# Kernel optimization log

Hardware: AMD Instinct MI355X
Metric: run time of the kernel (lower is better)

Reference implementation:

```python
import jax, jax.numpy as jnp
import numpy as np

EMB_DIM = 512
CATE1_CNT = 10
VOCAB = 100000
H_D = 1024
BN_EPS = 1e-5
NEG = -1e30  # masked value for max-pool


def setup_inputs() -> dict:
    key = jax.random.key(0)
    ks = jax.random.split(key, 12)
    B, LT, LD = 1024, 50, 200
    title = jax.random.randint(ks[0], (B, LT), 0, VOCAB, dtype=jnp.int64)
    desc = jax.random.randint(ks[1], (B, LD), 0, VOCAB, dtype=jnp.int64)
    t_len = jax.random.randint(ks[2], (B,), 1, LT + 1, dtype=jnp.int64)
    d_len = jax.random.randint(ks[3], (B,), 1, LD + 1, dtype=jnp.int64)
    emb = jax.random.normal(ks[4], (VOCAB, EMB_DIM), dtype=jnp.float32) * 0.02
    W_fc = jax.random.normal(ks[5], (4 * EMB_DIM, H_D), dtype=jnp.float32) * (1.0 / np.sqrt(4 * EMB_DIM))
    b_fc = jnp.zeros((H_D,), dtype=jnp.float32)
    gamma = jnp.ones((H_D,), dtype=jnp.float32)
    beta = jnp.zeros((H_D,), dtype=jnp.float32)
    W_clf = jax.random.normal(ks[6], (H_D, CATE1_CNT), dtype=jnp.float32) * (1.0 / np.sqrt(H_D))
    b_clf = jnp.zeros((CATE1_CNT,), dtype=jnp.float32)
    return {"title": title, "desc": desc, "t_len": t_len, "d_len": d_len,
            "emb": emb, "W_fc": W_fc, "b_fc": b_fc, "gamma": gamma,
            "beta": beta, "W_clf": W_clf, "b_clf": b_clf}


def _swem_pool(tokens, lens, emb):
    # tokens: [B, L] int, lens: [B] int -> (avg, max) each [B, D]
    e = emb[tokens]                                   # [B, L, D] gather
    L = tokens.shape[1]
    mask = (jnp.arange(L)[None, :] < lens[:, None])[..., None]  # [B, L, 1]
    s = jnp.sum(jnp.where(mask, e, 0.0), axis=1)      # [B, D]
    avg = s / jnp.maximum(lens, 1).astype(e.dtype)[:, None]
    mx = jnp.max(jnp.where(mask, e, NEG), axis=1)     # [B, D]
    return avg, mx


def reference(title, desc, t_len, d_len, emb, W_fc, b_fc, gamma, beta, W_clf, b_clf):
    t_avg, t_max = _swem_pool(title, t_len, emb)
    d_avg, d_max = _swem_pool(desc, d_len, emb)
    swem = jnp.concatenate([t_avg, t_max, d_avg, d_max], axis=-1)  # [B, 2048]
    h = swem @ W_fc + b_fc                                         # [B, H_D]
    # BatchNorm1d in training mode: batch statistics
    mean = jnp.mean(h, axis=0)
    var = jnp.var(h, axis=0)
    h = (h - mean) * jax.lax.rsqrt(var + BN_EPS) * gamma + beta
    h = jax.nn.relu(h)
    return h @ W_clf + b_clf                                       # [B, 10]
```

## Files before the change

### kernel.cpp

```cpp
#include <hip/hip_runtime.h>
#include <hip/hip_bf16.h>

#define EMB_DIM 512
#define B_SZ 1024
#define LT 50
#define LD 200
#define H_D 1024
#define K_FC 2048
#define NCLS 10
#define BN_EPS 1e-5f
#define NEGV -1e30f

typedef short short8 __attribute__((ext_vector_type(8)));
typedef float f32x4 __attribute__((ext_vector_type(4)));

#define SWZ(r, b) ((b) ^ (((r) & 7) << 4))

#define ACC4(S, M, E) \
  S.x += E.x; S.y += E.y; S.z += E.z; S.w += E.w; \
  M.x = fmaxf(M.x, E.x); M.y = fmaxf(M.y, E.y); \
  M.z = fmaxf(M.z, E.z); M.w = fmaxf(M.w, E.w);

__global__ __launch_bounds__(512) void pool_tr_kernel(
    const int* __restrict__ title, const int* __restrict__ desc,
    const int* __restrict__ t_len, const int* __restrict__ d_len,
    const float* __restrict__ emb, __hip_bfloat16* __restrict__ swem,
    const float* __restrict__ W, __hip_bfloat16* __restrict__ Wt,
    const float* __restrict__ Wclf, float* __restrict__ WclfT) {
  __shared__ float sm[8192];
  __shared__ int idxs[264];

  const int bid = blockIdx.x;
  const int tid = threadIdx.x;

  if (bid >= 2 * B_SZ) {
    const int t = bid - 2 * B_SZ;
    if (t == 512) {
      for (int idx = tid; idx < NCLS * H_D; idx += 512) {
        int j = idx >> 10, k = idx & 1023;
        WclfT[j * H_D + k] = Wclf[(size_t)k * NCLS + j];
      }
      return;
    }
    const int n0 = (t & 15) * 64;
    const int k0 = (t >> 4) * 64;
#pragma unroll
    for (int i = 0; i < 8; ++i) {
      int idx = i * 512 + tid;
      int r = idx >> 6, c = idx & 63;
      sm[r * 65 + c] = W[(size_t)(k0 + r) * H_D + n0 + c];
    }
    __syncthreads();
#pragma unroll
    for (int i = 0; i < 8; ++i) {
      int idx = i * 512 + tid;
      int r = idx >> 6, c = idx & 63;
      Wt[(size_t)(n0 + r) * K_FC + k0 + c] = __float2bfloat16(sm[c * 65 + r]);
    }
    return;
  }

  const int b = bid >> 1;
  const int half = bid & 1;
  const int wave = tid >> 6;
  const int lane = tid & 63;
  const int dbase = half * 256 + lane * 4;

  if (tid < LT) idxs[tid] = title[b * LT + tid];
  else if (tid >= 64 && tid < 64 + LD) idxs[tid] = desc[b * LD + tid - 64];
  const int tl = t_len[b];
  const int dl = d_len[b];
  __syncthreads();

#define POOL_LIST(LEN, IDXOFF, SARR, MARR)                                         \
  {                                                                                \
    float4 s0 = make_float4(0.f, 0.f, 0.f, 0.f), s1 = s0;                          \
    float4 m0 = make_float4(NEGV, NEGV, NEGV, NEGV), m1 = m0;                      \
    const int cnt = (LEN > wave) ? ((LEN - wave + 7) >> 3) : 0;                    \
    if (cnt >= 2) {                                                                \
      float4 e0 = *reinterpret_cast<const float4*>(                                \
          emb + (size_t)idxs[IDXOFF + wave] * EMB_DIM + dbase);                    \
      float4 e1 = *reinterpret_cast<const float4*>(                                \
          emb + (size_t)idxs[IDXOFF + wave + 8] * EMB_DIM + dbase);                \
      int i = 2;                                                                   \
      for (; i + 1 < cnt; i += 2) {                                                \
        float4 n0 = *reinterpret_cast<const float4*>(                              \
            emb + (size_t)idxs[IDXOFF + wave + i * 8] * EMB_DIM + dbase);          \
        float4 n1 = *reinterpret_cast<const float4*>(                              \
            emb + (size_t)idxs[IDXOFF + wave + (i + 1) * 8] * EMB_DIM + dbase);    \
        ACC4(s0, m0, e0); ACC4(s1, m1, e1);                                        \
        e0 = n0; e1 = n1;                                                          \
      }                                                                            \
      ACC4(s0, m0, e0); ACC4(s1, m1, e1);                                          \
      if (i < cnt) {                                                               \
        float4 t2 = *reinterpret_cast<const float4*>(                              \
            emb + (size_t)idxs[IDXOFF + wave + i * 8] * EMB_DIM + dbase);          \
        ACC4(s0, m0, t2);                                                          \
      }                                                                            \
    } else if (cnt == 1) {                                                         \
      float4 e0 = *reinterpret_cast<const float4*>(                                \
          emb + (size_t)idxs[IDXOFF + wave] * EMB_DIM + dbase);                    \
      ACC4(s0, m0, e0);                                                            \
    }                                                                              \
    s0.x += s1.x; s0.y += s1.y; s0.z += s1.z; s0.w += s1.w;                        \
    m0.x = fmaxf(m0.x, m1.x); m0.y = fmaxf(m0.y, m1.y);                            \
    m0.z = fmaxf(m0.z, m1.z); m0.w = fmaxf(m0.w, m1.w);                            \
    *reinterpret_cast<float4*>(&sm[(SARR * 8 + wave) * 256 + lane * 4]) = s0;      \
    *reinterpret_cast<float4*>(&sm[(MARR * 8 + wave) * 256 + lane * 4]) = m0;      \
  }

  POOL_LIST(tl, 0, 0, 1)
  POOL_LIST(dl, 64, 2, 3)

  __syncthreads();

  if (tid < 64) {
    const float it = 1.0f / (float)tl;
    const float id = 1.0f / (float)dl;
    float4 ts = make_float4(0.f, 0.f, 0.f, 0.f);
    float4 tm = make_float4(NEGV, NEGV, NEGV, NEGV);
    float4 ds = make_float4(0.f, 0.f, 0.f, 0.f);
    float4 dm = make_float4(NEGV, NEGV, NEGV, NEGV);
#pragma unroll
    for (int w = 0; w < 8; ++w) {
      float4 a = *reinterpret_cast<const float4*>(&sm[(0 * 8 + w) * 256 + tid * 4]);
      ts.x += a.x; ts.y += a.y; ts.z += a.z; ts.w += a.w;
      float4 bmx = *reinterpret_cast<const float4*>(&sm[(1 * 8 + w) * 256 + tid * 4]);
      tm.x = fmaxf(tm.x, bmx.x); tm.y = fmaxf(tm.y, bmx.y);
      tm.z = fmaxf(tm.z, bmx.z); tm.w = fmaxf(tm.w, bmx.w);
      float4 c = *reinterpret_cast<const float4*>(&sm[(2 * 8 + w) * 256 + tid * 4]);
      ds.x += c.x; ds.y += c.y; ds.z += c.z; ds.w += c.w;
      float4 dmx = *reinterpret_cast<const float4*>(&sm[(3 * 8 + w) * 256 + tid * 4]);
      dm.x = fmaxf(dm.x, dmx.x); dm.y = fmaxf(dm.y, dmx.y);
      dm.z = fmaxf(dm.z, dmx.z); dm.w = fmaxf(dm.w, dmx.w);
    }
    __hip_bfloat16* row = swem + (size_t)b * K_FC + half * 256 + tid * 4;
    union { ushort4 v; __hip_bfloat16 h[4]; } u;
    u.h[0] = __float2bfloat16(ts.x * it); u.h[1] = __float2bfloat16(ts.y * it);
    u.h[2] = __float2bfloat16(ts.z * it); u.h[3] = __float2bfloat16(ts.w * it);
    *reinterpret_cast<ushort4*>(&row[0 * EMB_DIM]) = u.v;
    u.h[0] = __float2bfloat16(tm.x); u.h[1] = __float2bfloat16(tm.y);
    u.h[2] = __float2bfloat16(tm.z); u.h[3] = __float2bfloat16(tm.w);
    *reinterpret_cast<ushort4*>(&row[1 * EMB_DIM]) = u.v;
    u.h[0] = __float2bfloat16(ds.x * id); u.h[1] = __float2bfloat16(ds.y * id);
    u.h[2] = __float2bfloat16(ds.z * id); u.h[3] = __float2bfloat16(ds.w * id);
    *reinterpret_cast<ushort4*>(&row[2 * EMB_DIM]) = u.v;
    u.h[0] = __float2bfloat16(dm.x); u.h[1] = __float2bfloat16(dm.y);
    u.h[2] = __float2bfloat16(dm.z); u.h[3] = __float2bfloat16(dm.w);
    *reinterpret_cast<ushort4*>(&row[3 * EMB_DIM]) = u.v;
  }
}

__global__ __launch_bounds__(512) void gemm_mfma_kernel(
    const __hip_bfloat16* __restrict__ A,
    const __hip_bfloat16* __restrict__ Bt,
    const float* __restrict__ bias, float* __restrict__ C,
    float* __restrict__ psum, float* __restrict__ psq) {
  __shared__ unsigned char As[2][8192];
  __shared__ unsigned char Bs[2][8192];
  __shared__ float reds[2][4][16];
  __shared__ float redq[2][4][16];
  const int tid = threadIdx.x;
  const int lane = tid & 63;
  const int wave = tid >> 6;
  const int wr = wave >> 2;
  const int wc = wave & 3;

  const int lin = blockIdx.y * 16 + blockIdx.x;
  const int swzb = (lin & 7) * 32 + (lin >> 3);
  const int bx = swzb & 15, by = swzb >> 4;
  const int m0 = by * 64, n0 = bx * 64;

  f32x4 acc[2] = {};

  const int rs = tid >> 3;
  const int os = tid & 7;
  const int hi = lane >> 4;
  const int lo = lane & 15;

  const __hip_bfloat16* pa = A + (size_t)(m0 + rs) * K_FC + os * 8;
  const __hip_bfloat16* pb = Bt + (size_t)(n0 + rs) * K_FC + os * 8;
  const int swz = SWZ(rs, rs * 128 + os * 16);

  float4 a1 = *reinterpret_cast<const float4*>(pa);
  float4 b1 = *reinterpret_cast<const float4*>(pb);
  *reinterpret_cast<float4*>(&As[0][swz]) = a1;
  *reinterpret_cast<float4*>(&Bs[0][swz]) = b1;
  a1 = *reinterpret_cast<const float4*>(pa + 64);
  b1 = *reinterpret_cast<const float4*>(pb + 64);
  __syncthreads();

  int cur = 0;
  for (int k0 = 0; k0 < K_FC; k0 += 64) {
    float4 an = make_float4(0.f, 0.f, 0.f, 0.f), bn = an;
    if (k0 + 128 < K_FC) {
      an = *reinterpret_cast<const float4*>(pa + k0 + 128);
      bn = *reinterpret_cast<const float4*>(pb + k0 + 128);
    }

#pragma unroll
    for (int kks = 0; kks < 2; ++kks) {
      short8 af[2];
#pragma unroll
      for (int mi = 0; mi < 2; ++mi) {
        int r = wr * 32 + mi * 16 + lo;
        af[mi] = *reinterpret_cast<const short8*>(&As[cur][SWZ(r, r * 128 + kks * 64 + hi * 16)]);
      }
      int rb = wc * 16 + lo;
      short8 bf = *reinterpret_cast<const short8*>(&Bs[cur][SWZ(rb, rb * 128 + kks * 64 + hi * 16)]);
#pragma unroll
      for (int mi = 0; mi < 2; ++mi)
        acc[mi] = __builtin_amdgcn_mfma_f32_16x16x32_bf16(af[mi], bf, acc[mi], 0, 0, 0);
    }

    if (k0 + 64 < K_FC) {
      *reinterpret_cast<float4*>(&As[cur ^ 1][swz]) = a1;
      *reinterpret_cast<float4*>(&Bs[cur ^ 1][swz]) = b1;
    }
    __syncthreads();
    a1 = an; b1 = bn;
    cur ^= 1;
  }

  {
    int col = n0 + wc * 16 + lo;
    float bv = bias[col];
    float s = 0.f, q = 0.f;
#pragma unroll
    for (int mi = 0; mi < 2; ++mi) {
#pragma unroll
      for (int r = 0; r < 4; ++r) {
        float v = acc[mi][r] + bv;
        s += v; q += v * v;
        int rowm = m0 + wr * 32 + mi * 16 + hi * 4 + r;
        C[(size_t)rowm * H_D + col] = v;
      }
    }
    s += __shfl_xor(s, 16);
    s += __shfl_xor(s, 32);
    q += __shfl_xor(q, 16);
    q += __shfl_xor(q, 32);
    if (lane < 16) { reds[wr][wc][lo] = s; redq[wr][wc][lo] = q; }
  }
  __syncthreads();
  if (tid < 64) {
    int wc2 = tid >> 4, lo2 = tid & 15;
    float s = reds[0][wc2][lo2] + reds[1][wc2][lo2];
    float q = redq[0][wc2][lo2] + redq[1][wc2][lo2];
    psum[by * H_D + n0 + tid] = s;
    psq[by * H_D + n0 + tid] = q;
  }
}

__global__ __launch_bounds__(256) void bn_final_kernel(
    const float* __restrict__ psum, const float* __restrict__ psq,
    const float* __restrict__ gamma, const float* __restrict__ beta,
    float* __restrict__ scale, float* __restrict__ shift) {
  const int col = blockIdx.x * 256 + threadIdx.x;
  float s = 0.f, q = 0.f;
#pragma unroll
  for (int i = 0; i < 16; ++i) {
    s += psum[i * H_D + col];
    q += psq[i * H_D + col];
  }
  const float inv_n = 1.0f / (float)B_SZ;
  float mean = s * inv_n;
  float var = q * inv_n - mean * mean;
  float rstd = rsqrtf(var + BN_EPS);
  float sc = rstd * gamma[col];
  scale[col] = sc;
  shift[col] = beta[col] - mean * sc;
}

__global__ __launch_bounds__(256) void clf_kernel(
    const float* __restrict__ h, const float* __restrict__ scale,
    const float* __restrict__ shift, const float* __restrict__ WT,
    const float* __restrict__ bclf, float* __restrict__ out) {
  __shared__ float v[H_D];
  const int row = blockIdx.x;
  const int tid = threadIdx.x;
#pragma unroll
  for (int i = 0; i < 4; ++i) {
    int k = tid + i * 256;
    float x = h[(size_t)row * H_D + k] * scale[k] + shift[k];
    v[k] = fmaxf(x, 0.f);
  }
  __syncthreads();
  const int wave = tid >> 6, lane = tid & 63;
  for (int j = wave; j < NCLS; j += 4) {
    const float* wrow = WT + j * H_D;
    float acc = 0.f;
#pragma unroll
    for (int i = 0; i < 16; ++i) {
      int k = lane + i * 64;
      acc += v[k] * wrow[k];
    }
#pragma unroll
    for (int off = 32; off > 0; off >>= 1) acc += __shfl_down(acc, off, 64);
    if (lane == 0) out[(size_t)row * NCLS + j] = acc + bclf[j];
  }
}

extern "C" void kernel_launch(void* const* d_in, const int* in_sizes, int n_in,
                              void* d_out, int out_size, void* d_ws, size_t ws_size,
                              hipStream_t stream) {
  const int* title = (const int*)d_in[0];
  const int* desc  = (const int*)d_in[1];
  const int* t_len = (const int*)d_in[2];
  const int* d_len = (const int*)d_in[3];
  const float* emb   = (const float*)d_in[4];
  const float* W_fc  = (const float*)d_in[5];
  const float* b_fc  = (const float*)d_in[6];
  const float* gamma = (const float*)d_in[7];
  const float* beta  = (const float*)d_in[8];
  const float* W_clf = (const float*)d_in[9];
  const float* b_clf = (const float*)d_in[10];
  float* out = (float*)d_out;

  unsigned char* ws = (unsigned char*)d_ws;
  __hip_bfloat16* swem = (__hip_bfloat16*)ws;
  __hip_bfloat16* Wt   = (__hip_bfloat16*)(ws + (4u << 20));
  float* h     = (float*)(ws + (8u << 20));
  float* psum  = (float*)(ws + (12u << 20));
  float* psq   = psum + 16 * H_D;
  float* scale = psq + 16 * H_D;
  float* shift = scale + H_D;
  float* WclfT = shift + H_D;

  const int n_tr_blocks = (K_FC / 64) * (H_D / 64) + 1;
  pool_tr_kernel<<<2 * B_SZ + n_tr_blocks, 512, 0, stream>>>(
      title, desc, t_len, d_len, emb, swem, W_fc, Wt, W_clf, WclfT);
  gemm_mfma_kernel<<<dim3(16, 16), 512, 0, stream>>>(swem, Wt, b_fc, h, psum, psq);
  bn_final_kernel<<<H_D / 256, 256, 0, stream>>>(psum, psq, gamma, beta, scale, shift);
  clf_kernel<<<B_SZ, 256, 0, stream>>>(h, scale, shift, WclfT, b_clf, out);
}
```

Baseline: 64.41 us.

## Halve GEMM tile width and fuse BN finalize into classifier kernel

The FC GEMM moves from 64x64 to 64x32 output tiles with 512 blocks, and each wave now computes a single 16x16 MFMA tile. This is meant to fill more compute units than the previous 256 blocks. The separate BN-finalize launch is removed. Each classifier block now recomputes scale and shift from the partial sums in shared memory and handles 4 rows per block. This trades one launch and a global round-trip for redundant per-block BN statistic work and lower MFMA reuse per wave.

```diff
diff --git a/kernel.cpp b/kernel.cpp
--- a/kernel.cpp
+++ b/kernel.cpp
@@ -157,37 +157,41 @@
     const float* __restrict__ bias, float* __restrict__ C,
     float* __restrict__ psum, float* __restrict__ psq) {
   __shared__ unsigned char As[2][8192];
-  __shared__ unsigned char Bs[2][8192];
-  __shared__ float reds[2][4][16];
-  __shared__ float redq[2][4][16];
+  __shared__ unsigned char Bs[2][4096];
+  __shared__ float reds[4][2][16];
+  __shared__ float redq[4][2][16];
   const int tid = threadIdx.x;
   const int lane = tid & 63;
   const int wave = tid >> 6;
-  const int wr = wave >> 2;
-  const int wc = wave & 3;
-
-  const int lin = blockIdx.y * 16 + blockIdx.x;
-  const int swzb = (lin & 7) * 32 + (lin >> 3);
-  const int bx = swzb & 15, by = swzb >> 4;
-  const int m0 = by * 64, n0 = bx * 64;
-
-  f32x4 acc[2] = {};
+  const int wr = wave & 3;
+  const int wcol = wave >> 2;
+
+  const int lin = blockIdx.y * 32 + blockIdx.x;
+  const int swzb = (lin & 7) * 64 + (lin >> 3);
+  const int bx = swzb & 31, by = swzb >> 5;
+  const int m0 = by * 64, n0 = bx * 32;
+
+  f32x4 acc = {};
 
   const int rs = tid >> 3;
   const int os = tid & 7;
   const int hi = lane >> 4;
   const int lo = lane & 15;
+  const bool doB = (tid < 256);
+  const int rsb = (tid >> 3) & 31;
 
   const __hip_bfloat16* pa = A + (size_t)(m0 + rs) * K_FC + os * 8;
-  const __hip_bfloat16* pb = Bt + (size_t)(n0 + rs) * K_FC + os * 8;
-  const int swz = SWZ(rs, rs * 128 + os * 16);
+  const __hip_bfloat16* pb = Bt + (size_t)(n0 + rsb) * K_FC + os * 8;
+  const int swzA = SWZ(rs, rs * 128 + os * 16);
+  const int swzB = SWZ(rsb, rsb * 128 + os * 16);
 
   float4 a1 = *reinterpret_cast<const float4*>(pa);
-  float4 b1 = *reinterpret_cast<const float4*>(pb);
-  *reinterpret_cast<float4*>(&As[0][swz]) = a1;
-  *reinterpret_cast<float4*>(&Bs[0][swz]) = b1;
+  float4 b1 = make_float4(0.f, 0.f, 0.f, 0.f);
+  if (doB) b1 = *reinterpret_cast<const float4*>(pb);
+  *reinterpret_cast<float4*>(&As[0][swzA]) = a1;
+  if (doB) *reinterpret_cast<float4*>(&Bs[0][swzB]) = b1;
   a1 = *reinterpret_cast<const float4*>(pa + 64);
-  b1 = *reinterpret_cast<const float4*>(pb + 64);
+  if (doB) b1 = *reinterpret_cast<const float4*>(pb + 64);
   __syncthreads();
 
   int cur = 0;
@@ -195,27 +199,21 @@
     float4 an = make_float4(0.f, 0.f, 0.f, 0.f), bn = an;
     if (k0 + 128 < K_FC) {
       an = *reinterpret_cast<const float4*>(pa + k0 + 128);
-      bn = *reinterpret_cast<const float4*>(pb + k0 + 128);
+      if (doB) bn = *reinterpret_cast<const float4*>(pb + k0 + 128);
     }
 
 #pragma unroll
     for (int kks = 0; kks < 2; ++kks) {
-      short8 af[2];
-#pragma unroll
-      for (int mi = 0; mi < 2; ++mi) {
-        int r = wr * 32 + mi * 16 + lo;
-        af[mi] = *reinterpret_cast<const short8*>(&As[cur][SWZ(r, r * 128 + kks * 64 + hi * 16)]);
-      }
-      int rb = wc * 16 + lo;
+      int r = wr * 16 + lo;
+      short8 af = *reinterpret_cast<const short8*>(&As[cur][SWZ(r, r * 128 + kks * 64 + hi * 16)]);
+      int rb = wcol * 16 + lo;
       short8 bf = *reinterpret_cast<const short8*>(&Bs[cur][SWZ(rb, rb * 128 + kks * 64 + hi * 16)]);
-#pragma unroll
-      for (int mi = 0; mi < 2; ++mi)
-        acc[mi] = __builtin_amdgcn_mfma_f32_16x16x32_bf16(af[mi], bf, acc[mi], 0, 0, 0);
+      acc = __builtin_amdgcn_mfma_f32_16x16x32_bf16(af, bf, acc, 0, 0, 0);
     }
 
     if (k0 + 64 < K_FC) {
-      *reinterpret_cast<float4*>(&As[cur ^ 1][swz]) = a1;
-      *reinterpret_cast<float4*>(&Bs[cur ^ 1][swz]) = b1;
+      *reinterpret_cast<float4*>(&As[cur ^ 1][swzA]) = a1;
+      if (doB) *reinterpret_cast<float4*>(&Bs[cur ^ 1][swzB]) = b1;
     }
     __syncthreads();
     a1 = an; b1 = bn;
@@ -223,81 +221,82 @@
   }
 
   {
-    int col = n0 + wc * 16 + lo;
+    int col = n0 + wcol * 16 + lo;
     float bv = bias[col];
     float s = 0.f, q = 0.f;
 #pragma unroll
-    for (int mi = 0; mi < 2; ++mi) {
-#pragma unroll
-      for (int r = 0; r < 4; ++r) {
-        float v = acc[mi][r] + bv;
-        s += v; q += v * v;
-        int rowm = m0 + wr * 32 + mi * 16 + hi * 4 + r;
-        C[(size_t)rowm * H_D + col] = v;
-      }
+    for (int r = 0; r < 4; ++r) {
+      float v = acc[r] + bv;
+      s += v; q += v * v;
+      int rowm = m0 + wr * 16 + hi * 4 + r;
+      C[(size_t)rowm * H_D + col] = v;
     }
     s += __shfl_xor(s, 16);
     s += __shfl_xor(s, 32);
     q += __shfl_xor(q, 16);
     q += __shfl_xor(q, 32);
-    if (lane < 16) { reds[wr][wc][lo] = s; redq[wr][wc][lo] = q; }
-  }
-  __syncthreads();
-  if (tid < 64) {
+    if (lane < 16) { reds[wr][wcol][lo] = s; redq[wr][wcol][lo] = q; }
+  }
+  __syncthreads();
+  if (tid < 32) {
     int wc2 = tid >> 4, lo2 = tid & 15;
-    float s = reds[0][wc2][lo2] + reds[1][wc2][lo2];
-    float q = redq[0][wc2][lo2] + redq[1][wc2][lo2];
+    float s = reds[0][wc2][lo2] + reds[1][wc2][lo2] + reds[2][wc2][lo2] + reds[3][wc2][lo2];
+    float q = redq[0][wc2][lo2] + redq[1][wc2][lo2] + redq[2][wc2][lo2] + redq[3][wc2][lo2];
     psum[by * H_D + n0 + tid] = s;
     psq[by * H_D + n0 + tid] = q;
   }
 }
 
-__global__ __launch_bounds__(256) void bn_final_kernel(
-    const float* __restrict__ psum, const float* __restrict__ psq,
-    const float* __restrict__ gamma, const float* __restrict__ beta,
-    float* __restrict__ scale, float* __restrict__ shift) {
-  const int col = blockIdx.x * 256 + threadIdx.x;
-  float s = 0.f, q = 0.f;
-#pragma unroll
-  for (int i = 0; i < 16; ++i) {
-    s += psum[i * H_D + col];
-    q += psq[i * H_D + col];
-  }
-  const float inv_n = 1.0f / (float)B_SZ;
-  float mean = s * inv_n;
-  float var = q * inv_n - mean * mean;
-  float rstd = rsqrtf(var + BN_EPS);
-  float sc = rstd * gamma[col];
-  scale[col] = sc;
-  shift[col] = beta[col] - mean * sc;
-}
-
-__global__ __launch_bounds__(256) void clf_kernel(
-    const float* __restrict__ h, const float* __restrict__ scale,
-    const float* __restrict__ shift, const float* __restrict__ WT,
+__global__ __launch_bounds__(512) void clf_kernel(
+    const float* __restrict__ h, const float* __restrict__ psum,
+    const float* __restrict__ psq, const float* __restrict__ gamma,
+    const float* __restrict__ beta, const float* __restrict__ WT,
     const float* __restrict__ bclf, float* __restrict__ out) {
-  __shared__ float v[H_D];
-  const int row = blockIdx.x;
+  __shared__ float scl[H_D];
+  __shared__ float sft[H_D];
+  __shared__ float v4[4][H_D];
   const int tid = threadIdx.x;
-#pragma unroll
-  for (int i = 0; i < 4; ++i) {
-    int k = tid + i * 256;
-    float x = h[(size_t)row * H_D + k] * scale[k] + shift[k];
-    v[k] = fmaxf(x, 0.f);
-  }
-  __syncthreads();
+
+  for (int c = tid; c < H_D; c += 512) {
+    float s = 0.f, q = 0.f;
+#pragma unroll
+    for (int i = 0; i < 16; ++i) {
+      s += psum[i * H_D + c];
+      q += psq[i * H_D + c];
+    }
+    const float inv_n = 1.0f / (float)B_SZ;
+    float mean = s * inv_n;
+    float var = q * inv_n - mean * mean;
+    float rstd = rsqrtf(var + BN_EPS);
+    float sc = rstd * gamma[c];
+    scl[c] = sc;
+    sft[c] = beta[c] - mean * sc;
+  }
+  __syncthreads();
+
+  const int r0 = blockIdx.x * 4;
+#pragma unroll
+  for (int r = 0; r < 4; ++r) {
+    for (int k = tid; k < H_D; k += 512) {
+      float x = h[(size_t)(r0 + r) * H_D + k] * scl[k] + sft[k];
+      v4[r][k] = fmaxf(x, 0.f);
+    }
+  }
+  __syncthreads();
+
   const int wave = tid >> 6, lane = tid & 63;
-  for (int j = wave; j < NCLS; j += 4) {
+  for (int p = wave; p < 4 * NCLS; p += 8) {
+    const int r = p / NCLS, j = p % NCLS;
     const float* wrow = WT + j * H_D;
     float acc = 0.f;
 #pragma unroll
     for (int i = 0; i < 16; ++i) {
       int k = lane + i * 64;
-      acc += v[k] * wrow[k];
+      acc += v4[r][k] * wrow[k];
     }
 #pragma unroll
     for (int off = 32; off > 0; off >>= 1) acc += __shfl_down(acc, off, 64);
-    if (lane == 0) out[(size_t)row * NCLS + j] = acc + bclf[j];
+    if (lane == 0) out[(size_t)(r0 + r) * NCLS + j] = acc + bclf[j];
   }
 }
 
@@ -323,14 +322,11 @@
   float* h     = (float*)(ws + (8u << 20));
   float* psum  = (float*)(ws + (12u << 20));
   float* psq   = psum + 16 * H_D;
-  float* scale = psq + 16 * H_D;
-  float* shift = scale + H_D;
-  float* WclfT = shift + H_D;
+  float* WclfT = psq + 16 * H_D;
 
   const int n_tr_blocks = (K_FC / 64) * (H_D / 64) + 1;
   pool_tr_kernel<<<2 * B_SZ + n_tr_blocks, 512, 0, stream>>>(
       title, desc, t_len, d_len, emb, swem, W_fc, Wt, W_clf, WclfT);
-  gemm_mfma_kernel<<<dim3(16, 16), 512, 0, stream>>>(swem, Wt, b_fc, h, psum, psq);
-  bn_final_kernel<<<H_D / 256, 256, 0, stream>>>(psum, psq, gamma, beta, scale, shift);
-  clf_kernel<<<B_SZ, 256, 0, stream>>>(h, scale, shift, WclfT, b_clf, out);
+  gemm_mfma_kernel<<<dim3(32, 16), 512, 0, stream>>>(swem, Wt, b_fc, h, psum, psq);
+  clf_kernel<<<B_SZ / 4, 512, 0, stream>>>(h, psum, psq, gamma, beta, WclfT, b_clf, out);
 }
```

Measured after the change: 72.72 us. 12.9% more time.
